# Optimization experiments

Measured on AMD Instinct MI355X. Metric: run time of the kernel, lower is better.

Reference implementation:

```python
import jax, jax.numpy as jnp
import numpy as np

B, S, IN, H, C = 4, 1024, 1024, 256, 8

def setup_inputs() -> dict:
    key = jax.random.key(0)
    ks = jax.random.split(key, 9)
    scale_in = 1.0 / np.sqrt(IN)
    scale_h2 = 1.0 / np.sqrt(2 * H)
    return {
        "seq_feats": jax.random.normal(ks[0], (B, S, IN), dtype=jnp.float32),
        "U": jax.random.normal(ks[1], (H, C, H), dtype=jnp.float32) * 0.02,
        "W_weight": jax.random.uniform(ks[2], (C, 2 * H), minval=-scale_h2, maxval=scale_h2, dtype=jnp.float32),
        "W_bias": jax.random.uniform(ks[3], (C,), minval=-scale_h2, maxval=scale_h2, dtype=jnp.float32),
        "start_w": jax.random.uniform(ks[4], (H, IN), minval=-scale_in, maxval=scale_in, dtype=jnp.float32),
        "start_b": jax.random.uniform(ks[5], (H,), minval=-scale_in, maxval=scale_in, dtype=jnp.float32),
        "end_w": jax.random.uniform(ks[6], (H, IN), minval=-scale_in, maxval=scale_in, dtype=jnp.float32),
        "end_b": jax.random.uniform(ks[7], (H,), minval=-scale_in, maxval=scale_in, dtype=jnp.float32),
    }

def reference(seq_feats, U, W_weight, W_bias, start_w, start_b, end_w, end_b):
    # Hs, He: [b, s, h]
    Hs = jnp.einsum('bsi,hi->bsh', seq_feats, start_w) + start_b
    He = jnp.einsum('bsi,hi->bsh', seq_feats, end_w) + end_b
    # biaffine: [b, s, e, c]
    biaff = jnp.einsum('bsh,hcg,beg->bsec', Hs, U, He)
    # Linear over concat([Hs_repeat, He_repeat]) == split-weight broadcast sum
    Ws, We = W_weight[:, :256], W_weight[:, 256:]
    lin = (jnp.einsum('bsh,ch->bsc', Hs, Ws)[:, :, None, :]
           + jnp.einsum('beh,ch->bec', He, We)[:, None, :, :]
           + W_bias)
    return biaff + lin
```

## Files before the change

### kernel.cpp

```cpp
#include <hip/hip_runtime.h>
#include <stdint.h>


#define BDIM 256

typedef float f32x4 __attribute__((ext_vector_type(4)));
typedef __bf16 bf16x8 __attribute__((ext_vector_type(8)));
typedef unsigned int u32;
typedef unsigned short u16;
typedef const __attribute__((address_space(1))) u32* gas_ptr;
typedef __attribute__((address_space(3))) u32* las_ptr;

static __device__ __forceinline__ void load_lds16(const void* g, void* l) {
  __builtin_amdgcn_global_load_lds((gas_ptr)g, (las_ptr)l, 16, 0, 0);
}

static __device__ __forceinline__ u16 f32_to_bf16(float f) {
  union { float f; u32 u; } v; v.f = f;
  u32 r = v.u + 0x7FFFu + ((v.u >> 16) & 1u);
  return (u16)(r >> 16);
}
static __device__ __forceinline__ u32 pack_bf16(float lo, float hi) {
  return (u32)f32_to_bf16(lo) | ((u32)f32_to_bf16(hi) << 16);
}
static __device__ __forceinline__ float bf16lo_to_f32(u32 u) {
  union { u32 u; float f; } v; v.u = u << 16;
  return v.f;
}
static __device__ __forceinline__ float bf16hi_to_f32(u32 u) {
  union { u32 u; float f; } v; v.u = u & 0xFFFF0000u;
  return v.f;
}

static __device__ __forceinline__ void stage32(u16* lds, int dst, const u16* src,
                                               int srow, int ld, int kcol, int tid) {
  const int r = tid >> 3;
  const int sl = tid & 7;
  load_lds16(src + (size_t)(srow + r) * ld + kcol + ((sl ^ (r & 7)) << 3),
             &lds[dst + tid * 8]);
}

static __device__ __forceinline__ void stage32_f32(u16* lds, int dst, const float* src,
                                                   int srow, int ld, int kcol, int tid) {
  const int r = tid >> 3;
  const int sl = tid & 7;
  const float* p = src + (size_t)(srow + r) * ld + kcol + ((sl ^ (r & 7)) << 3);
  const float4 v0 = *reinterpret_cast<const float4*>(p);
  const float4 v1 = *reinterpret_cast<const float4*>(p + 4);
  uint4 w;
  w.x = pack_bf16(v0.x, v0.y);
  w.y = pack_bf16(v0.z, v0.w);
  w.z = pack_bf16(v1.x, v1.y);
  w.w = pack_bf16(v1.z, v1.w);
  *reinterpret_cast<uint4*>(&lds[dst + tid * 8]) = w;
}

static __device__ __forceinline__ bf16x8 rd64(const u16* lds, int base, int row, int kslot) {
  return *reinterpret_cast<const bf16x8*>(&lds[base + row * 64 + ((kslot ^ (row & 7)) << 3)]);
}

__global__ __launch_bounds__(BDIM, 4)
void k1p(const float* __restrict__ seq,
         const float* __restrict__ sw,
         const float* __restrict__ ew,
         const float* __restrict__ U,
         const float* __restrict__ sb,
         const float* __restrict__ eb,
         u16* __restrict__ Hboth,
         u16* __restrict__ Ut)
{
  const int tid = threadIdx.x;
  const int bid = blockIdx.x;

  if (bid >= 512) {
    const int i = (bid - 512) * 1024 + tid * 4;
    const int n = i >> 8;
    const int h = i & 255;
    ushort4 o;
    o.x = f32_to_bf16(U[(size_t)(h + 0) * 2048 + n]);
    o.y = f32_to_bf16(U[(size_t)(h + 1) * 2048 + n]);
    o.z = f32_to_bf16(U[(size_t)(h + 2) * 2048 + n]);
    o.w = f32_to_bf16(U[(size_t)(h + 3) * 2048 + n]);
    *reinterpret_cast<ushort4*>(Ut + i) = o;
    return;
  }

  __shared__ u16 lds[2 * 4096];

  const int lane = tid & 63;
  const int wv   = tid >> 6;
  const int wr   = wv >> 1;
  const int wq   = wv & 1;
  const int rA   = lane & 15;
  const int kq   = lane >> 4;

  int id = bid;
  id = (id & 7) * 64 + (id >> 3);
  const int n0 = (id & 7) * 64;
  const int m0 = (id >> 3) * 64;

  const float* wsrc = (n0 < 256) ? (sw + (size_t)n0 * 1024)
                                 : (ew + (size_t)(n0 - 256) * 1024);

  f32x4 acc[2][2];
#pragma unroll
  for (int i = 0; i < 2; ++i)
#pragma unroll
    for (int j = 0; j < 2; ++j) acc[i][j] = (f32x4)0.f;

#pragma unroll 1
  for (int kt = 0; kt < 1024; kt += 64) {
    stage32_f32(lds, 0,           seq,  m0,      1024, kt, tid);
    stage32_f32(lds, 2048,        seq,  m0 + 32, 1024, kt, tid);
    stage32_f32(lds, 4096,        wsrc, 0,       1024, kt, tid);
    stage32_f32(lds, 4096 + 2048, wsrc, 32,      1024, kt, tid);
    __syncthreads();

    bf16x8 aF[2][2], bF[2][2];
#pragma unroll
    for (int mi = 0; mi < 2; ++mi)
#pragma unroll
      for (int ks = 0; ks < 2; ++ks)
        aF[mi][ks] = rd64(lds, 0, wr * 32 + mi * 16 + rA, (ks << 2) | kq);
#pragma unroll
    for (int ni = 0; ni < 2; ++ni)
#pragma unroll
      for (int ks = 0; ks < 2; ++ks)
        bF[ni][ks] = rd64(lds, 4096, wq * 32 + ni * 16 + rA, (ks << 2) | kq);
#pragma unroll
    for (int mi = 0; mi < 2; ++mi)
#pragma unroll
      for (int ni = 0; ni < 2; ++ni)
#pragma unroll
        for (int ks = 0; ks < 2; ++ks)
          acc[mi][ni] = __builtin_amdgcn_mfma_f32_16x16x32_bf16(
              aF[mi][ks], bF[ni][ks], acc[mi][ni], 0, 0, 0);
    __syncthreads();
  }

#pragma unroll
  for (int mi = 0; mi < 2; ++mi) {
#pragma unroll
    for (int ni = 0; ni < 2; ++ni) {
      const int n = n0 + wq * 32 + ni * 16 + rA;
      const float bn = (n < 256) ? sb[n] : eb[n - 256];
      const int mr = m0 + wr * 32 + mi * 16 + kq * 4;
#pragma unroll
      for (int r = 0; r < 4; ++r)
        Hboth[(size_t)(mr + r) * 512 + n] = f32_to_bf16(acc[mi][ni][r] + bn);
    }
  }
}

__global__ __launch_bounds__(BDIM, 2)
void k2lin(const u16* __restrict__ Hboth,
           const u16* __restrict__ Utbf,
           u16* __restrict__ Tbf,
           const float* __restrict__ Ww,
           const float* __restrict__ Wb,
           float* __restrict__ linS,
           float* __restrict__ linE)
{
  const int bid = blockIdx.x;
  const int tid = threadIdx.x;

  if (bid >= 512) {
    const int idx = (bid - 512) * BDIM + tid;
    const int m = idx >> 3;
    const int c = idx & 7;
    const uint4* hs4 = reinterpret_cast<const uint4*>(Hboth + (size_t)m * 512);
    const uint4* he4 = reinterpret_cast<const uint4*>(Hboth + (size_t)m * 512 + 256);
    const float* wsp = Ww + c * 512;
    const float* wep = wsp + 256;
    float s1 = 0.f, s2 = 0.f;
#pragma unroll 4
    for (int t = 0; t < 32; ++t) {
      const uint4 a = hs4[t];
      const uint4 b = he4[t];
      const u32 aw[4] = {a.x, a.y, a.z, a.w};
      const u32 bw[4] = {b.x, b.y, b.z, b.w};
#pragma unroll
      for (int q = 0; q < 4; ++q) {
        const int h = t * 8 + q * 2;
        s1 += bf16lo_to_f32(aw[q]) * wsp[h] + bf16hi_to_f32(aw[q]) * wsp[h + 1];
        s2 += bf16lo_to_f32(bw[q]) * wep[h] + bf16hi_to_f32(bw[q]) * wep[h + 1];
      }
    }
    linS[idx] = s1;
    linE[idx] = s2 + Wb[c];
    return;
  }

  __shared__ u16 lds[2 * 8192];

  int id = bid;
  id = (id & 7) * 64 + (id >> 3);
  const int n0 = (id & 15) * 128;
  const int m0 = (id >> 4) * 128;

  const int lane = tid & 63;
  const int wv   = tid >> 6;
  const int wr   = wv >> 1;
  const int wc   = wv & 1;
  const int rA   = lane & 15;
  const int kq   = lane >> 4;

  f32x4 acc[4][4];
#pragma unroll
  for (int i = 0; i < 4; ++i)
#pragma unroll
    for (int j = 0; j < 4; ++j) acc[i][j] = (f32x4)0.f;

#pragma unroll 1
  for (int kt = 0; kt < 256; kt += 64) {
#pragma unroll
    for (int h = 0; h < 4; ++h)
      stage32(lds, h * 2048, Hboth, m0 + h * 32, 512, kt, tid);
#pragma unroll
    for (int h = 0; h < 4; ++h)
      stage32(lds, 8192 + h * 2048, Utbf, n0 + h * 32, 256, kt, tid);
    __syncthreads();

    bf16x8 aF[4][2], bF[4][2];
#pragma unroll
    for (int mi = 0; mi < 4; ++mi)
#pragma unroll
      for (int ks = 0; ks < 2; ++ks)
        aF[mi][ks] = rd64(lds, 0, wr * 64 + mi * 16 + rA, (ks << 2) | kq);
#pragma unroll
    for (int ni = 0; ni < 4; ++ni)
#pragma unroll
      for (int ks = 0; ks < 2; ++ks)
        bF[ni][ks] = rd64(lds, 8192, wc * 64 + ni * 16 + rA, (ks << 2) | kq);
#pragma unroll
    for (int mi = 0; mi < 4; ++mi)
#pragma unroll
      for (int ni = 0; ni < 4; ++ni)
#pragma unroll
        for (int ks = 0; ks < 2; ++ks)
          acc[mi][ni] = __builtin_amdgcn_mfma_f32_16x16x32_bf16(
              aF[mi][ks], bF[ni][ks], acc[mi][ni], 0, 0, 0);
    __syncthreads();
  }

#pragma unroll
  for (int mi = 0; mi < 4; ++mi) {
#pragma unroll
    for (int ni = 0; ni < 4; ++ni) {
      const int mBase = m0 + wr * 64 + mi * 16 + kq * 4;
      const int n = n0 + wc * 64 + ni * 16 + rA;
#pragma unroll
      for (int r = 0; r < 4; ++r)
        Tbf[(size_t)(mBase + r) * 2048 + n] = f32_to_bf16(acc[mi][ni][r]);
    }
  }
}

__global__ __launch_bounds__(BDIM, 4)
void gemm128_biaff(const u16* __restrict__ Tall,
                   const u16* __restrict__ Bg,
                   float* __restrict__ Out,
                   const float* __restrict__ linSall,
                   const float* __restrict__ linEall)
{
  __shared__ u16 lds[2 * 8192];

  const int tid  = threadIdx.x;
  const int lane = tid & 63;
  const int wv   = tid >> 6;
  const int wr   = wv >> 1;
  const int wc   = wv & 1;
  const int rA   = lane & 15;
  const int kq   = lane >> 4;
  const int z    = blockIdx.z;

  int id = blockIdx.y * gridDim.x + blockIdx.x;
  id = (id & 7) * 64 + (id >> 3);
  const int n0 = (id & 7) * 128;
  const int m0 = (id >> 3) * 128;

  const u16* Ag  = Tall + (size_t)z * (8192 * 256);
  const u16* Bgz = Bg   + (size_t)z * (1024 * 512);

  f32x4 acc[4][4];
#pragma unroll
  for (int i = 0; i < 4; ++i)
#pragma unroll
    for (int j = 0; j < 4; ++j) acc[i][j] = (f32x4)0.f;

#pragma unroll 1
  for (int kt = 0; kt < 256; kt += 64) {
#pragma unroll
    for (int h = 0; h < 4; ++h)
      stage32(lds, h * 2048, Ag, m0 + h * 32, 256, kt, tid);
#pragma unroll
    for (int h = 0; h < 4; ++h)
      stage32(lds, 8192 + h * 2048, Bgz, n0 + h * 32, 512, kt, tid);
    __syncthreads();

    bf16x8 aF[4][2], bF[4][2];
#pragma unroll
    for (int mi = 0; mi < 4; ++mi)
#pragma unroll
      for (int ks = 0; ks < 2; ++ks)
        aF[mi][ks] = rd64(lds, 0, wr * 64 + mi * 16 + rA, (ks << 2) | kq);
#pragma unroll
    for (int ni = 0; ni < 4; ++ni)
#pragma unroll
      for (int ks = 0; ks < 2; ++ks)
        bF[ni][ks] = rd64(lds, 8192, wc * 64 + ni * 16 + rA, (ks << 2) | kq);
#pragma unroll
    for (int mi = 0; mi < 4; ++mi)
#pragma unroll
      for (int ni = 0; ni < 4; ++ni)
#pragma unroll
        for (int ks = 0; ks < 2; ++ks)
          acc[mi][ni] = __builtin_amdgcn_mfma_f32_16x16x32_bf16(
              aF[mi][ks], bF[ni][ks], acc[mi][ni], 0, 0, 0);
    __syncthreads();
  }

  float* OutZ = Out + (size_t)z * 8388608;
  const float* lS = linSall + (size_t)z * 8192;
  const float* lE = linEall + (size_t)z * 8192;
#pragma unroll
  for (int mi = 0; mi < 4; ++mi) {
#pragma unroll
    for (int ni = 0; ni < 4; ++ni) {
      const int mBase = m0 + wr * 64 + mi * 16 + kq * 4;
      const int e = n0 + wc * 64 + ni * 16 + rA;
      const int s = mBase >> 3;
      const int c0 = mBase & 7;
      const float4 ls4 = *reinterpret_cast<const float4*>(lS + mBase);
      const float4 le4 = *reinterpret_cast<const float4*>(lE + (e << 3) + c0);
      float4 o;
      o.x = acc[mi][ni][0] + ls4.x + le4.x;
      o.y = acc[mi][ni][1] + ls4.y + le4.y;
      o.z = acc[mi][ni][2] + ls4.z + le4.z;
      o.w = acc[mi][ni][3] + ls4.w + le4.w;
      *reinterpret_cast<float4*>(OutZ + ((size_t)s << 13) + ((size_t)e << 3) + c0) = o;
    }
  }
}

extern "C" void kernel_launch(void* const* d_in, const int* in_sizes, int n_in,
                              void* d_out, int out_size, void* d_ws, size_t ws_size,
                              hipStream_t stream)
{
  const float* seq = (const float*)d_in[0];
  const float* U   = (const float*)d_in[1];
  const float* Ww  = (const float*)d_in[2];
  const float* Wb  = (const float*)d_in[3];
  const float* sw  = (const float*)d_in[4];
  const float* sb  = (const float*)d_in[5];
  const float* ew  = (const float*)d_in[6];
  const float* eb  = (const float*)d_in[7];
  float* out = (float*)d_out;

  u16* Utbf  = (u16*)d_ws;
  u16* Hboth = Utbf + 524288;
  u16* Tbf   = Hboth + 2097152;
  float* linS = (float*)(Tbf + 8388608);
  float* linE = linS + 32768;

  k1p<<<1024, BDIM, 0, stream>>>(seq, sw, ew, U, sb, eb, Hboth, Utbf);

  k2lin<<<640, BDIM, 0, stream>>>(Hboth, Utbf, Tbf, Ww, Wb, linS, linE);

  gemm128_biaff<<<dim3(8, 64, 4), BDIM, 0, stream>>>(
      Tbf, Hboth + 256, out, linS, linE);
}
```

Baseline: 82.20 us.

## Double-buffer LDS staging in biaffine GEMM with manual vmcnt waits

Doubles the LDS buffer of the biaffine GEMM kernel so the next 64-wide K tile is staged through global_load_lds while MFMAs run on the current one. Synchronisation now uses explicit s_waitcnt vmcnt counts and raw s_barrier calls with sched_barrier instead of __syncthreads. The per-row linear-term loads are hoisted before the main loop so their latency overlaps the GEMM. In exchange, LDS use doubles and launch bounds drop from 4 to 2 blocks per CU. With only four K iterations, there is little loop for the overlap to amortise over.

```diff
diff --git a/kernel.cpp b/kernel.cpp
--- a/kernel.cpp
+++ b/kernel.cpp
@@ -256,14 +256,23 @@
   }
 }
 
-__global__ __launch_bounds__(BDIM, 4)
+#define K3STAGE(buf, t) do {                                                   \
+    _Pragma("unroll")                                                          \
+    for (int h = 0; h < 4; ++h)                                                \
+      stage32(lds, (buf) * 16384 + h * 2048, Ag, m0 + h * 32, 256, (t) * 64, tid); \
+    _Pragma("unroll")                                                          \
+    for (int h = 0; h < 4; ++h)                                                \
+      stage32(lds, (buf) * 16384 + 8192 + h * 2048, Bgz, n0 + h * 32, 512, (t) * 64, tid); \
+  } while (0)
+
+__global__ __launch_bounds__(BDIM, 2)
 void gemm128_biaff(const u16* __restrict__ Tall,
                    const u16* __restrict__ Bg,
                    float* __restrict__ Out,
                    const float* __restrict__ linSall,
                    const float* __restrict__ linEall)
 {
-  __shared__ u16 lds[2 * 8192];
+  __shared__ u16 lds[4 * 8192];
 
   const int tid  = threadIdx.x;
   const int lane = tid & 63;
@@ -288,27 +297,37 @@
 #pragma unroll
     for (int j = 0; j < 4; ++j) acc[i][j] = (f32x4)0.f;
 
-#pragma unroll 1
-  for (int kt = 0; kt < 256; kt += 64) {
-#pragma unroll
-    for (int h = 0; h < 4; ++h)
-      stage32(lds, h * 2048, Ag, m0 + h * 32, 256, kt, tid);
-#pragma unroll
-    for (int h = 0; h < 4; ++h)
-      stage32(lds, 8192 + h * 2048, Bgz, n0 + h * 32, 512, kt, tid);
-    __syncthreads();
+  const float* lS = linSall + (size_t)z * 8192;
+  float4 ls4[4];
+#pragma unroll
+  for (int mi = 0; mi < 4; ++mi)
+    ls4[mi] = *reinterpret_cast<const float4*>(lS + m0 + wr * 64 + mi * 16 + kq * 4);
+
+  K3STAGE(0, 0);
+
+#pragma unroll
+  for (int t = 0; t < 4; ++t) {
+    const int cur = t & 1;
+    if (t < 3) {
+      K3STAGE(cur ^ 1, t + 1);
+      asm volatile("s_waitcnt vmcnt(8)" ::: "memory");
+    } else {
+      asm volatile("s_waitcnt vmcnt(0)" ::: "memory");
+    }
+    __builtin_amdgcn_sched_barrier(0);
+    __builtin_amdgcn_s_barrier();
 
     bf16x8 aF[4][2], bF[4][2];
 #pragma unroll
     for (int mi = 0; mi < 4; ++mi)
 #pragma unroll
       for (int ks = 0; ks < 2; ++ks)
-        aF[mi][ks] = rd64(lds, 0, wr * 64 + mi * 16 + rA, (ks << 2) | kq);
+        aF[mi][ks] = rd64(lds, cur * 16384, wr * 64 + mi * 16 + rA, (ks << 2) | kq);
 #pragma unroll
     for (int ni = 0; ni < 4; ++ni)
 #pragma unroll
       for (int ks = 0; ks < 2; ++ks)
-        bF[ni][ks] = rd64(lds, 8192, wc * 64 + ni * 16 + rA, (ks << 2) | kq);
+        bF[ni][ks] = rd64(lds, cur * 16384 + 8192, wc * 64 + ni * 16 + rA, (ks << 2) | kq);
 #pragma unroll
     for (int mi = 0; mi < 4; ++mi)
 #pragma unroll
@@ -317,11 +336,12 @@
         for (int ks = 0; ks < 2; ++ks)
           acc[mi][ni] = __builtin_amdgcn_mfma_f32_16x16x32_bf16(
               aF[mi][ks], bF[ni][ks], acc[mi][ni], 0, 0, 0);
-    __syncthreads();
+
+    __builtin_amdgcn_sched_barrier(0);
+    __builtin_amdgcn_s_barrier();
   }
 
   float* OutZ = Out + (size_t)z * 8388608;
-  const float* lS = linSall + (size_t)z * 8192;
   const float* lE = linEall + (size_t)z * 8192;
 #pragma unroll
   for (int mi = 0; mi < 4; ++mi) {
@@ -331,13 +351,12 @@
       const int e = n0 + wc * 64 + ni * 16 + rA;
       const int s = mBase >> 3;
       const int c0 = mBase & 7;
-      const float4 ls4 = *reinterpret_cast<const float4*>(lS + mBase);
       const float4 le4 = *reinterpret_cast<const float4*>(lE + (e << 3) + c0);
       float4 o;
-      o.x = acc[mi][ni][0] + ls4.x + le4.x;
-      o.y = acc[mi][ni][1] + ls4.y + le4.y;
-      o.z = acc[mi][ni][2] + ls4.z + le4.z;
-      o.w = acc[mi][ni][3] + ls4.w + le4.w;
+      o.x = acc[mi][ni][0] + ls4[mi].x + le4.x;
+      o.y = acc[mi][ni][1] + ls4[mi].y + le4.y;
+      o.z = acc[mi][ni][2] + ls4[mi].z + le4.z;
+      o.w = acc[mi][ni][3] + ls4[mi].w + le4.w;
       *reinterpret_cast<float4*>(OutZ + ((size_t)s << 13) + ((size_t)e << 3) + c0) = o;
     }
   }
```

Result: no change. 80.77 us (-1.7%).
